# Kernel optimization log

Measured on AMD Instinct MI355X. Metric: run time of the kernel, lower is better.

## Reference

```python
import jax, jax.numpy as jnp
import numpy as np


def gcn_conv(x, src, dst, norm, W, b, n_nodes):
    # PyG GCNConv: out[dst] = sum_edges norm * (x @ W)[src] + b
    h = x @ W                      # [N, F_out]
    msg = h[src] * norm[:, None]   # [E', F_out] gather + scale
    out = jax.ops.segment_sum(msg, dst, num_segments=n_nodes)
    return out + b


def _gcn_norm(edge_index, n_nodes):
    # add self loops, compute symmetric normalization deg^-1/2[src]*deg^-1/2[dst]
    loop = jnp.arange(n_nodes, dtype=edge_index.dtype)
    src = jnp.concatenate([edge_index[0], loop])
    dst = jnp.concatenate([edge_index[1], loop])
    deg = jnp.zeros((n_nodes,), jnp.float32).at[dst].add(1.0)
    dinv = jnp.where(deg > 0, jax.lax.rsqrt(deg), 0.0)
    norm = dinv[src] * dinv[dst]
    return src, dst, norm


def setup_inputs() -> dict:
    key = jax.random.key(0)
    ks = jax.random.split(key, 5)
    N, E, C_in, C_out = 50000, 800000, 128, 32
    H = 2 * C_out
    x = jax.random.normal(ks[0], (N, C_in), jnp.float32)
    edge_index = jax.random.randint(ks[1], (2, E), 0, N, jnp.int64)
    s1 = 1.0 / np.sqrt(C_in)
    s2 = 1.0 / np.sqrt(H)
    W1 = jax.random.uniform(ks[2], (C_in, H), jnp.float32, -s1, s1)
    b1 = jnp.zeros((H,), jnp.float32)
    W_mu = jax.random.uniform(ks[3], (H, C_out), jnp.float32, -s2, s2)
    b_mu = jnp.zeros((C_out,), jnp.float32)
    W_ls = jax.random.uniform(ks[4], (H, C_out), jnp.float32, -s2, s2)
    b_ls = jnp.zeros((C_out,), jnp.float32)
    return {"x": x, "edge_index": edge_index, "W1": W1, "b1": b1,
            "W_mu": W_mu, "b_mu": b_mu, "W_ls": W_ls, "b_ls": b_ls}


def reference(x, edge_index, W1, b1, W_mu, b_mu, W_ls, b_ls):
    n_nodes = x.shape[0]
    src, dst, norm = _gcn_norm(edge_index, n_nodes)
    h = jax.nn.relu(gcn_conv(x, src, dst, norm, W1, b1, n_nodes))
    mu = gcn_conv(h, src, dst, norm, W_mu, b_mu, n_nodes)
    logstd = gcn_conv(h, src, dst, norm, W_ls, b_ls, n_nodes)
    return mu, logstd
```

## Files before the change

kernel.cpp:

```cpp
#include <hip/hip_runtime.h>
#include <hip/hip_fp16.h>
#include <math.h>


typedef unsigned int uint;
typedef unsigned short ushort;
typedef __attribute__((ext_vector_type(8))) short short8;
typedef __attribute__((ext_vector_type(4))) float f32x4;
typedef __attribute__((ext_vector_type(2))) float f32v2;

__device__ __forceinline__ ushort f2bf(float x) {
    uint u = __float_as_uint(x);
    u += 0x7fffu + ((u >> 16) & 1u);
    return (ushort)(u >> 16);
}
__device__ __forceinline__ float bf2f(ushort h) {
    return __uint_as_float((uint)h << 16);
}

__global__ __launch_bounds__(256) void k_hist(
        const int* __restrict__ dst, int* __restrict__ bcount, int E) {
    __shared__ int h[256];
    const int tid = threadIdx.x;
    h[tid] = 0;
    __syncthreads();
    const int base = blockIdx.x * 2048;
    #pragma unroll
    for (int k = 0; k < 8; ++k) {
        int i = base + k * 256 + tid;
        if (i < E) {
            int d = __builtin_nontemporal_load(dst + i);
            atomicAdd(&h[d >> 8], 1);
        }
    }
    __syncthreads();
    if (h[tid]) atomicAdd(&bcount[tid], h[tid]);
}

__global__ __launch_bounds__(256) void k_bscan(
        const int* __restrict__ bcount, int* __restrict__ bbase,
        int* __restrict__ bcursor, int E) {
    __shared__ int p[256];
    const int t = threadIdx.x;
    int v = bcount[t];
    p[t] = v;
    __syncthreads();
    #pragma unroll
    for (int off = 1; off < 256; off <<= 1) {
        int x = (t >= off) ? p[t - off] : 0;
        __syncthreads();
        p[t] += x;
        __syncthreads();
    }
    int excl = p[t] - v;
    bbase[t] = excl;
    bcursor[t] = excl;
    if (t == 255) bbase[256] = p[255];
}

__global__ __launch_bounds__(256) void k_scatterA(
        const int* __restrict__ src, const int* __restrict__ dst,
        int* __restrict__ bcursor, uint* __restrict__ recs, int E) {
    __shared__ int h[256];
    __shared__ int rb[256];
    const int tid = threadIdx.x;
    h[tid] = 0;
    __syncthreads();
    const int base = blockIdx.x * 2048;
    uint rec[8]; int rk[8];
    #pragma unroll
    for (int k = 0; k < 8; ++k) {
        int i = base + k * 256 + tid;
        if (i < E) {
            int s = __builtin_nontemporal_load(src + i);
            int d = __builtin_nontemporal_load(dst + i);
            int b = d >> 8;
            rec[k] = (uint)s | ((uint)(d & 255) << 16) | ((uint)b << 24);
            rk[k] = atomicAdd(&h[b], 1);
        }
    }
    __syncthreads();
    rb[tid] = h[tid] ? atomicAdd(&bcursor[tid], h[tid]) : 0;
    __syncthreads();
    #pragma unroll
    for (int k = 0; k < 8; ++k) {
        int i = base + k * 256 + tid;
        if (i < E) recs[rb[rec[k] >> 24] + rk[k]] = rec[k];
    }
}

__global__ __launch_bounds__(256) void k_phaseB(
        const uint* __restrict__ recs, const int* __restrict__ bbase,
        int* __restrict__ row_ptr, float* __restrict__ dinv,
        ushort* __restrict__ edges, int N, int E, int NBUCK) {
    __shared__ int h[256];
    __shared__ int p[256];
    const int tid = threadIdx.x;
    const int b = blockIdx.x;
    const int base = bbase[b];
    const int cnt  = bbase[b + 1] - base;
    h[tid] = 0;
    __syncthreads();
    for (int i = tid; i < cnt; i += 256)
        atomicAdd(&h[(recs[base + i] >> 16) & 255], 1);
    __syncthreads();
    int v = h[tid];
    p[tid] = v;
    __syncthreads();
    #pragma unroll
    for (int off = 1; off < 256; off <<= 1) {
        int x = (tid >= off) ? p[tid - off] : 0;
        __syncthreads();
        p[tid] += x;
        __syncthreads();
    }
    const int excl = p[tid] - v;
    const int node = b * 256 + tid;
    if (node < N) {
        row_ptr[node] = base + excl;
        dinv[node] = rsqrtf((float)(v + 1));
    }
    if (b == NBUCK - 1 && tid == 0) row_ptr[N] = E;
    h[tid] = excl;
    __syncthreads();
    for (int i = tid; i < cnt; i += 256) {
        uint r = recs[base + i];
        int dl = (r >> 16) & 255;
        int pos = atomicAdd(&h[dl], 1);
        edges[base + pos] = (ushort)(r & 0xffffu);
    }
}

__global__ __launch_bounds__(256, 4) void k_gemm(
        const float* __restrict__ x, const float* __restrict__ W1,
        const float* __restrict__ dinv, ushort* __restrict__ hp, int N) {
    const int tid = threadIdx.x;
    const int w = tid >> 6, l = tid & 63;
    const int m = l & 15, q = l >> 4;
    const int row0 = blockIdx.x * 64 + w * 16;
    const size_t arow = (size_t)min(row0 + m, N - 1);
    f32x4 acc0 = {0.f, 0.f, 0.f, 0.f}, acc1 = acc0, acc2 = acc0, acc3 = acc0;
    #pragma unroll
    for (int kc = 0; kc < 4; ++kc) {
        const int kofs = kc * 32 + q * 8;
        const float4* xr = (const float4*)(x + arow * 128 + kofs);
        float4 xa = xr[0], xb = xr[1];
        short8 a;
        a[0] = (short)f2bf(xa.x); a[1] = (short)f2bf(xa.y);
        a[2] = (short)f2bf(xa.z); a[3] = (short)f2bf(xa.w);
        a[4] = (short)f2bf(xb.x); a[5] = (short)f2bf(xb.y);
        a[6] = (short)f2bf(xb.z); a[7] = (short)f2bf(xb.w);
        short8 b0, b1, b2, b3;
        #pragma unroll
        for (int i = 0; i < 8; ++i) {
            const float* wk = W1 + (size_t)(kofs + i) * 64 + m;
            b0[i] = (short)f2bf(wk[0]);
            b1[i] = (short)f2bf(wk[16]);
            b2[i] = (short)f2bf(wk[32]);
            b3[i] = (short)f2bf(wk[48]);
        }
        acc0 = __builtin_amdgcn_mfma_f32_16x16x32_bf16(a, b0, acc0, 0, 0, 0);
        acc1 = __builtin_amdgcn_mfma_f32_16x16x32_bf16(a, b1, acc1, 0, 0, 0);
        acc2 = __builtin_amdgcn_mfma_f32_16x16x32_bf16(a, b2, acc2, 0, 0, 0);
        acc3 = __builtin_amdgcn_mfma_f32_16x16x32_bf16(a, b3, acc3, 0, 0, 0);
    }
    #pragma unroll
    for (int r = 0; r < 4; ++r) {
        int row = row0 + q * 4 + r;
        if (row >= N) continue;
        float dv = dinv[row];
        ushort* hr = hp + (size_t)row * 64 + m;
        hr[0]  = f2bf(acc0[r] * dv);
        hr[16] = f2bf(acc1[r] * dv);
        hr[32] = f2bf(acc2[r] * dv);
        hr[48] = f2bf(acc3[r] * dv);
    }
}

__device__ __forceinline__ f32v2 gather_rows(
        const uint* __restrict__ hp, const ushort* __restrict__ edges,
        int beg, int end, int E, int lane, int hl, int half) {
    f32v2 acc = {0.f, 0.f};
    for (int base = beg; base < end; base += 64) {
        int cnt = end - base; if (cnt > 64) cnt = 64;
        int mrec = (int)edges[min(base + lane, E - 1)];
        int steps = (cnt + 1) >> 1;
        for (int t = 0; t < steps; t += 8) {
            if (2 * t + 16 <= cnt) {
                #pragma unroll
                for (int i = 0; i < 8; ++i) {
                    int r = __shfl(mrec, 2 * (t + i) + half);
                    uint v = hp[(size_t)r * 32 + hl];
                    f32v2 vf;
                    vf.x = __uint_as_float(v << 16);
                    vf.y = __uint_as_float(v & 0xffff0000u);
                    acc = acc + vf;
                }
            } else {
                #pragma unroll
                for (int i = 0; i < 8; ++i) {
                    int e = 2 * (t + i) + half;
                    int r = __shfl(mrec, min(e, cnt - 1));
                    uint v = hp[(size_t)r * 32 + hl];
                    v = (e < cnt) ? v : 0u;
                    f32v2 vf;
                    vf.x = __uint_as_float(v << 16);
                    vf.y = __uint_as_float(v & 0xffff0000u);
                    acc = acc + vf;
                }
            }
        }
    }
    acc.x += __shfl_xor(acc.x, 32);
    acc.y += __shfl_xor(acc.y, 32);
    return acc;
}

__global__ __launch_bounds__(256, 8) void k_gather1(
        const uint* __restrict__ hp, const int* __restrict__ row_ptr,
        const ushort* __restrict__ edges, const float* __restrict__ dinv,
        const float* __restrict__ b1, uint* __restrict__ ho, int N, int E) {
    const int lane = threadIdx.x & 63;
    const int hl = lane & 31, half = lane >> 5;
    const int n = blockIdx.x * 4 + (threadIdx.x >> 6);
    if (n >= N) return;
    const int beg = row_ptr[n], end = row_ptr[n + 1];
    f32v2 acc = gather_rows(hp, edges, beg, end, E, lane, hl, half);
    if (half == 0) {
        const float dv = dinv[n];
        const uint sv = hp[(size_t)n * 32 + hl];
        const float2 b = ((const float2*)b1)[hl];
        float s0 = acc.x + bf2f((ushort)sv);
        float s1 = acc.y + bf2f((ushort)(sv >> 16));
        float h0 = fmaxf(fmaf(dv, s0, b.x), 0.f) * dv;
        float h1 = fmaxf(fmaf(dv, s1, b.y), 0.f) * dv;
        ho[(size_t)n * 32 + hl] = (uint)f2bf(h0) | ((uint)f2bf(h1) << 16);
    }
}

__global__ __launch_bounds__(256, 8) void k_gather2(
        const uint* __restrict__ hp, const int* __restrict__ row_ptr,
        const ushort* __restrict__ edges, const float* __restrict__ dinv,
        const float* __restrict__ Wmu, const float* __restrict__ Wls,
        const float* __restrict__ bmu, const float* __restrict__ bls,
        float* __restrict__ out, int N, int E) {
    __shared__ float hs[4][64];
    const int lane = threadIdx.x & 63;
    const int hl = lane & 31, half = lane >> 5;
    const int w = threadIdx.x >> 6;
    const int n = blockIdx.x * 4 + w;
    if (n >= N) return;
    const int beg = row_ptr[n], end = row_ptr[n + 1];
    f32v2 acc = gather_rows(hp, edges, beg, end, E, lane, hl, half);
    if (half == 0) {
        const float dv = dinv[n];
        const uint sv = hp[(size_t)n * 32 + hl];
        float g0 = dv * (acc.x + bf2f((ushort)sv));
        float g1 = dv * (acc.y + bf2f((ushort)(sv >> 16)));
        float2 p; p.x = g0; p.y = g1;
        *(float2*)&hs[w][2 * hl] = p;
    }
    const float* Wsel = (lane < 32) ? (Wmu + lane) : (Wls + (lane - 32));
    const float bias  = (lane < 32) ? bmu[lane] : bls[lane - 32];
    float c0 = 0.f, c1 = 0.f, c2 = 0.f, c3 = 0.f;
    #pragma unroll 4
    for (int k = 0; k < 64; k += 4) {
        c0 = fmaf(hs[w][k + 0], Wsel[(k + 0) * 32], c0);
        c1 = fmaf(hs[w][k + 1], Wsel[(k + 1) * 32], c1);
        c2 = fmaf(hs[w][k + 2], Wsel[(k + 2) * 32], c2);
        c3 = fmaf(hs[w][k + 3], Wsel[(k + 3) * 32], c3);
    }
    float t = (c0 + c1) + (c2 + c3) + bias;
    if (lane < 32) out[(size_t)n * 32 + lane] = t;
    else           out[(size_t)N * 32 + (size_t)n * 32 + (lane - 32)] = t;
}

extern "C" void kernel_launch(void* const* d_in, const int* in_sizes, int n_in,
                              void* d_out, int out_size, void* d_ws, size_t ws_size,
                              hipStream_t stream) {
    const float* x   = (const float*)d_in[0];
    const int*   ei  = (const int*)d_in[1];
    const float* W1  = (const float*)d_in[2];
    const float* b1  = (const float*)d_in[3];
    const float* Wmu = (const float*)d_in[4];
    const float* bmu = (const float*)d_in[5];
    const float* Wls = (const float*)d_in[6];
    const float* bls = (const float*)d_in[7];
    float* out = (float*)d_out;

    const int N = in_sizes[0] / 128;
    const int E = in_sizes[1] / 2;
    const int* src = ei;
    const int* dst = ei + E;
    const int HB    = (E + 2047) / 2048;
    const int NBUCK = (N + 255) / 256;
    const int GB    = (N + 63) / 64;
    const int NG    = (N + 3) / 4;

    char* w = (char*)d_ws;
    auto carve = [&](size_t bytes) { char* p = w; w += (bytes + 1023) & ~(size_t)1023; return p; };
    int*    bcount  = (int*)   carve(256 * 4);
    int*    bbase   = (int*)   carve(257 * 4);
    int*    bcursor = (int*)   carve(256 * 4);
    uint*   recs    = (uint*)  carve((size_t)E * 4);
    int*    row_ptr = (int*)   carve((size_t)(N + 1) * 4);
    float*  dinv    = (float*) carve((size_t)N * 4);
    ushort* edges   = (ushort*)carve((size_t)E * 2);
    ushort* h_pre   = (ushort*)carve((size_t)N * 64 * 2);
    ushort* h_mid   = (ushort*)carve((size_t)N * 64 * 2);

    hipMemsetAsync(bcount, 0, 256 * 4, stream);
    k_hist    <<<HB, 256, 0, stream>>>(dst, bcount, E);
    k_bscan   <<<1, 256, 0, stream>>>(bcount, bbase, bcursor, E);
    k_scatterA<<<HB, 256, 0, stream>>>(src, dst, bcursor, recs, E);
    k_phaseB  <<<NBUCK, 256, 0, stream>>>(recs, bbase, row_ptr, dinv, edges, N, E, NBUCK);
    k_gemm    <<<GB, 256, 0, stream>>>(x, W1, dinv, h_pre, N);
    k_gather1 <<<NG, 256, 0, stream>>>((const uint*)h_pre, row_ptr, edges, dinv,
                                       b1, (uint*)h_mid, N, E);
    k_gather2 <<<NG, 256, 0, stream>>>((const uint*)h_mid, row_ptr, edges, dinv,
                                       Wmu, Wls, bmu, bls, out, N, E);
}
```

Measured before the change: 194.8 us.

## Fuse GEMM with dst histogram and apply dinv scaling inside phaseB

The first-layer GEMM no longer depends on dinv, so it is merged into one launch with the destination histogram kernel, with blocks split by index. The dinv row scaling of the GEMM output moves into phaseB, which rescales its bucket's rows in place after building the CSR. The aim is to cut one launch and let the independent GEMM and histogram work overlap. It also adds nontemporal loads and stores in the gather kernels. The cost is an extra read-modify-write pass over h_pre and a second bf16 rounding step.

```diff
diff --git a/kernel.cpp b/kernel.cpp
--- a/kernel.cpp
+++ b/kernel.cpp
@@ -18,123 +18,28 @@
     return __uint_as_float((uint)h << 16);
 }
 
-__global__ __launch_bounds__(256) void k_hist(
+__global__ __launch_bounds__(256, 4) void k_gemm_hist(
+        const float* __restrict__ x, const float* __restrict__ W1,
+        ushort* __restrict__ hp, int N, int GB,
         const int* __restrict__ dst, int* __restrict__ bcount, int E) {
-    __shared__ int h[256];
     const int tid = threadIdx.x;
-    h[tid] = 0;
-    __syncthreads();
-    const int base = blockIdx.x * 2048;
-    #pragma unroll
-    for (int k = 0; k < 8; ++k) {
-        int i = base + k * 256 + tid;
-        if (i < E) {
-            int d = __builtin_nontemporal_load(dst + i);
-            atomicAdd(&h[d >> 8], 1);
+    if (blockIdx.x >= GB) {
+        __shared__ int h[256];
+        h[tid] = 0;
+        __syncthreads();
+        const int base = (blockIdx.x - GB) * 2048;
+        #pragma unroll
+        for (int k = 0; k < 8; ++k) {
+            int i = base + k * 256 + tid;
+            if (i < E) {
+                int d = __builtin_nontemporal_load(dst + i);
+                atomicAdd(&h[d >> 8], 1);
+            }
         }
-    }
-    __syncthreads();
-    if (h[tid]) atomicAdd(&bcount[tid], h[tid]);
-}
-
-__global__ __launch_bounds__(256) void k_bscan(
-        const int* __restrict__ bcount, int* __restrict__ bbase,
-        int* __restrict__ bcursor, int E) {
-    __shared__ int p[256];
-    const int t = threadIdx.x;
-    int v = bcount[t];
-    p[t] = v;
-    __syncthreads();
-    #pragma unroll
-    for (int off = 1; off < 256; off <<= 1) {
-        int x = (t >= off) ? p[t - off] : 0;
-        __syncthreads();
-        p[t] += x;
-        __syncthreads();
-    }
-    int excl = p[t] - v;
-    bbase[t] = excl;
-    bcursor[t] = excl;
-    if (t == 255) bbase[256] = p[255];
-}
-
-__global__ __launch_bounds__(256) void k_scatterA(
-        const int* __restrict__ src, const int* __restrict__ dst,
-        int* __restrict__ bcursor, uint* __restrict__ recs, int E) {
-    __shared__ int h[256];
-    __shared__ int rb[256];
-    const int tid = threadIdx.x;
-    h[tid] = 0;
-    __syncthreads();
-    const int base = blockIdx.x * 2048;
-    uint rec[8]; int rk[8];
-    #pragma unroll
-    for (int k = 0; k < 8; ++k) {
-        int i = base + k * 256 + tid;
-        if (i < E) {
-            int s = __builtin_nontemporal_load(src + i);
-            int d = __builtin_nontemporal_load(dst + i);
-            int b = d >> 8;
-            rec[k] = (uint)s | ((uint)(d & 255) << 16) | ((uint)b << 24);
-            rk[k] = atomicAdd(&h[b], 1);
-        }
-    }
-    __syncthreads();
-    rb[tid] = h[tid] ? atomicAdd(&bcursor[tid], h[tid]) : 0;
-    __syncthreads();
-    #pragma unroll
-    for (int k = 0; k < 8; ++k) {
-        int i = base + k * 256 + tid;
-        if (i < E) recs[rb[rec[k] >> 24] + rk[k]] = rec[k];
-    }
-}
-
-__global__ __launch_bounds__(256) void k_phaseB(
-        const uint* __restrict__ recs, const int* __restrict__ bbase,
-        int* __restrict__ row_ptr, float* __restrict__ dinv,
-        ushort* __restrict__ edges, int N, int E, int NBUCK) {
-    __shared__ int h[256];
-    __shared__ int p[256];
-    const int tid = threadIdx.x;
-    const int b = blockIdx.x;
-    const int base = bbase[b];
-    const int cnt  = bbase[b + 1] - base;
-    h[tid] = 0;
-    __syncthreads();
-    for (int i = tid; i < cnt; i += 256)
-        atomicAdd(&h[(recs[base + i] >> 16) & 255], 1);
-    __syncthreads();
-    int v = h[tid];
-    p[tid] = v;
-    __syncthreads();
-    #pragma unroll
-    for (int off = 1; off < 256; off <<= 1) {
-        int x = (tid >= off) ? p[tid - off] : 0;
-        __syncthreads();
-        p[tid] += x;
-        __syncthreads();
-    }
-    const int excl = p[tid] - v;
-    const int node = b * 256 + tid;
-    if (node < N) {
-        row_ptr[node] = base + excl;
-        dinv[node] = rsqrtf((float)(v + 1));
-    }
-    if (b == NBUCK - 1 && tid == 0) row_ptr[N] = E;
-    h[tid] = excl;
-    __syncthreads();
-    for (int i = tid; i < cnt; i += 256) {
-        uint r = recs[base + i];
-        int dl = (r >> 16) & 255;
-        int pos = atomicAdd(&h[dl], 1);
-        edges[base + pos] = (ushort)(r & 0xffffu);
-    }
-}
-
-__global__ __launch_bounds__(256, 4) void k_gemm(
-        const float* __restrict__ x, const float* __restrict__ W1,
-        const float* __restrict__ dinv, ushort* __restrict__ hp, int N) {
-    const int tid = threadIdx.x;
+        __syncthreads();
+        if (h[tid]) atomicAdd(&bcount[tid], h[tid]);
+        return;
+    }
     const int w = tid >> 6, l = tid & 63;
     const int m = l & 15, q = l >> 4;
     const int row0 = blockIdx.x * 64 + w * 16;
@@ -168,12 +73,119 @@
     for (int r = 0; r < 4; ++r) {
         int row = row0 + q * 4 + r;
         if (row >= N) continue;
-        float dv = dinv[row];
         ushort* hr = hp + (size_t)row * 64 + m;
-        hr[0]  = f2bf(acc0[r] * dv);
-        hr[16] = f2bf(acc1[r] * dv);
-        hr[32] = f2bf(acc2[r] * dv);
-        hr[48] = f2bf(acc3[r] * dv);
+        hr[0]  = f2bf(acc0[r]);
+        hr[16] = f2bf(acc1[r]);
+        hr[32] = f2bf(acc2[r]);
+        hr[48] = f2bf(acc3[r]);
+    }
+}
+
+__global__ __launch_bounds__(256) void k_bscan(
+        const int* __restrict__ bcount, int* __restrict__ bbase,
+        int* __restrict__ bcursor, int E) {
+    __shared__ int p[256];
+    const int t = threadIdx.x;
+    int v = bcount[t];
+    p[t] = v;
+    __syncthreads();
+    #pragma unroll
+    for (int off = 1; off < 256; off <<= 1) {
+        int x = (t >= off) ? p[t - off] : 0;
+        __syncthreads();
+        p[t] += x;
+        __syncthreads();
+    }
+    int excl = p[t] - v;
+    bbase[t] = excl;
+    bcursor[t] = excl;
+    if (t == 255) bbase[256] = p[255];
+}
+
+__global__ __launch_bounds__(256) void k_scatterA(
+        const int* __restrict__ src, const int* __restrict__ dst,
+        int* __restrict__ bcursor, uint* __restrict__ recs, int E) {
+    __shared__ int h[256];
+    __shared__ int rb[256];
+    const int tid = threadIdx.x;
+    h[tid] = 0;
+    __syncthreads();
+    const int base = blockIdx.x * 2048;
+    uint rec[8]; int rk[8];
+    #pragma unroll
+    for (int k = 0; k < 8; ++k) {
+        int i = base + k * 256 + tid;
+        if (i < E) {
+            int s = __builtin_nontemporal_load(src + i);
+            int d = __builtin_nontemporal_load(dst + i);
+            int b = d >> 8;
+            rec[k] = (uint)s | ((uint)(d & 255) << 16) | ((uint)b << 24);
+            rk[k] = atomicAdd(&h[b], 1);
+        }
+    }
+    __syncthreads();
+    rb[tid] = h[tid] ? atomicAdd(&bcursor[tid], h[tid]) : 0;
+    __syncthreads();
+    #pragma unroll
+    for (int k = 0; k < 8; ++k) {
+        int i = base + k * 256 + tid;
+        if (i < E) recs[rb[rec[k] >> 24] + rk[k]] = rec[k];
+    }
+}
+
+__global__ __launch_bounds__(256) void k_phaseB(
+        const uint* __restrict__ recs, const int* __restrict__ bbase,
+        int* __restrict__ row_ptr, float* __restrict__ dinv,
+        ushort* __restrict__ edges, uint* __restrict__ hp,
+        int N, int E, int NBUCK) {
+    __shared__ int h[256];
+    __shared__ int p[256];
+    __shared__ float sdv[256];
+    const int tid = threadIdx.x;
+    const int b = blockIdx.x;
+    const int base = bbase[b];
+    const int cnt  = bbase[b + 1] - base;
+    h[tid] = 0;
+    __syncthreads();
+    for (int i = tid; i < cnt; i += 256)
+        atomicAdd(&h[(recs[base + i] >> 16) & 255], 1);
+    __syncthreads();
+    int v = h[tid];
+    p[tid] = v;
+    __syncthreads();
+    #pragma unroll
+    for (int off = 1; off < 256; off <<= 1) {
+        int x = (tid >= off) ? p[tid - off] : 0;
+        __syncthreads();
+        p[tid] += x;
+        __syncthreads();
+    }
+    const int excl = p[tid] - v;
+    const float dv = rsqrtf((float)(v + 1));
+    sdv[tid] = dv;
+    const int node = b * 256 + tid;
+    if (node < N) {
+        row_ptr[node] = base + excl;
+        dinv[node] = dv;
+    }
+    if (b == NBUCK - 1 && tid == 0) row_ptr[N] = E;
+    h[tid] = excl;
+    __syncthreads();
+    for (int i = tid; i < cnt; i += 256) {
+        uint r = recs[base + i];
+        int dl = (r >> 16) & 255;
+        int pos = atomicAdd(&h[dl], 1);
+        edges[base + pos] = (ushort)(r & 0xffffu);
+    }
+    const int rows = min(256, N - b * 256);
+    if (rows <= 0) return;
+    uint* hpb = hp + (size_t)b * 256 * 32;
+    for (int idx = tid; idx < rows * 32; idx += 256) {
+        float d2 = sdv[idx >> 5];
+        uint w = hpb[idx];
+        float lo = bf2f((ushort)w) * d2;
+        float hi = bf2f((ushort)(w >> 16)) * d2;
+        hpb[idx] = (uint)f2bf(lo) | ((uint)f2bf(hi) << 16);
     }
 }
 
@@ -183,7 +195,7 @@
     f32v2 acc = {0.f, 0.f};
     for (int base = beg; base < end; base += 64) {
         int cnt = end - base; if (cnt > 64) cnt = 64;
-        int mrec = (int)edges[min(base + lane, E - 1)];
+        int mrec = (int)__builtin_nontemporal_load(edges + min(base + lane, E - 1));
         int steps = (cnt + 1) >> 1;
         for (int t = 0; t < steps; t += 8) {
             if (2 * t + 16 <= cnt) {
@@ -234,7 +246,8 @@
         float s1 = acc.y + bf2f((ushort)(sv >> 16));
         float h0 = fmaxf(fmaf(dv, s0, b.x), 0.f) * dv;
         float h1 = fmaxf(fmaf(dv, s1, b.y), 0.f) * dv;
-        ho[(size_t)n * 32 + hl] = (uint)f2bf(h0) | ((uint)f2bf(h1) << 16);
+        uint pk = (uint)f2bf(h0) | ((uint)f2bf(h1) << 16);
+        __builtin_nontemporal_store(pk, ho + (size_t)n * 32 + hl);
     }
 }
 
@@ -271,8 +284,8 @@
         c3 = fmaf(hs[w][k + 3], Wsel[(k + 3) * 32], c3);
     }
     float t = (c0 + c1) + (c2 + c3) + bias;
-    if (lane < 32) out[(size_t)n * 32 + lane] = t;
-    else           out[(size_t)N * 32 + (size_t)n * 32 + (lane - 32)] = t;
+    if (lane < 32) __builtin_nontemporal_store(t, out + (size_t)n * 32 + lane);
+    else __builtin_nontemporal_store(t, out + (size_t)N * 32 + (size_t)n * 32 + (lane - 32));
 }
 
 extern "C" void kernel_launch(void* const* d_in, const int* in_sizes, int n_in,
@@ -306,17 +319,17 @@
     int*    row_ptr = (int*)   carve((size_t)(N + 1) * 4);
     float*  dinv    = (float*) carve((size_t)N * 4);
     ushort* edges   = (ushort*)carve((size_t)E * 2);
-    ushort* h_pre   = (ushort*)carve((size_t)N * 64 * 2);
+    ushort* h_pre   = (ushort*)carve((size_t)NBUCK * 256 * 64 * 2);
     ushort* h_mid   = (ushort*)carve((size_t)N * 64 * 2);
 
     hipMemsetAsync(bcount, 0, 256 * 4, stream);
-    k_hist    <<<HB, 256, 0, stream>>>(dst, bcount, E);
-    k_bscan   <<<1, 256, 0, stream>>>(bcount, bbase, bcursor, E);
-    k_scatterA<<<HB, 256, 0, stream>>>(src, dst, bcursor, recs, E);
-    k_phaseB  <<<NBUCK, 256, 0, stream>>>(recs, bbase, row_ptr, dinv, edges, N, E, NBUCK);
-    k_gemm    <<<GB, 256, 0, stream>>>(x, W1, dinv, h_pre, N);
-    k_gather1 <<<NG, 256, 0, stream>>>((const uint*)h_pre, row_ptr, edges, dinv,
-                                       b1, (uint*)h_mid, N, E);
-    k_gather2 <<<NG, 256, 0, stream>>>((const uint*)h_mid, row_ptr, edges, dinv,
-                                       Wmu, Wls, bmu, bls, out, N, E);
-}
+    k_gemm_hist<<<GB + HB, 256, 0, stream>>>(x, W1, h_pre, N, GB, dst, bcount, E);
+    k_bscan    <<<1, 256, 0, stream>>>(bcount, bbase, bcursor, E);
+    k_scatterA <<<HB, 256, 0, stream>>>(src, dst, bcursor, recs, E);
+    k_phaseB   <<<NBUCK, 256, 0, stream>>>(recs, bbase, row_ptr, dinv, edges,
+                                           (uint*)h_pre, N, E, NBUCK);
+    k_gather1  <<<NG, 256, 0, stream>>>((const uint*)h_pre, row_ptr, edges, dinv,
+                                        b1, (uint*)h_mid, N, E);
+    k_gather2  <<<NG, 256, 0, stream>>>((const uint*)h_mid, row_ptr, edges, dinv,
+                                        Wmu, Wls, bmu, bls, out, N, E);
+}
```

Result: slower. 199.7 us (+2.6%).
